# Performance work log

Hardware: AMD Instinct MI355X
Metric: run time of the kernel (lower is better)

Reference implementation:

```python
import jax, jax.numpy as jnp
import numpy as np

B, S, H = 1, 2000, 4096
NH, NKV, HD = 32, 8, 128
NREP = NH // NKV
ROPE_THETA = 10000.0
RES_LEN = 128          # kv_residual_len
K_BITS = V_BITS = 4
K_GROUP = V_GROUP = 64
NEG = -1e9


def setup_inputs() -> dict:
    key = jax.random.key(0)
    ks = jax.random.split(key, 6)
    hidden_states = jax.random.normal(ks[0], (B, S, H), jnp.float32) * 0.02
    wq = jax.random.normal(ks[1], (H, NH * HD), jnp.float32) * (H ** -0.5)
    wk = jax.random.normal(ks[2], (H, NKV * HD), jnp.float32) * (H ** -0.5)
    wv = jax.random.normal(ks[3], (H, NKV * HD), jnp.float32) * (H ** -0.5)
    wo = jax.random.normal(ks[4], (NH * HD, H), jnp.float32) * (H ** -0.5)
    position_ids = jnp.broadcast_to(jnp.arange(S, dtype=jnp.int64), (B, S))
    causal = jnp.tril(jnp.ones((S, S), dtype=bool))
    attention_mask = jnp.where(causal, 0.0, NEG).astype(jnp.float32)[None, None]  # [1,1,S,S]
    return {"hidden_states": hidden_states, "wq": wq, "wk": wk, "wv": wv,
            "wo": wo, "position_ids": position_ids, "attention_mask": attention_mask}


def _rotate_half(x):
    x1, x2 = jnp.split(x, 2, axis=-1)
    return jnp.concatenate([-x2, x1], axis=-1)


def _rope_cos_sin(position_ids):
    inv_freq = 1.0 / (ROPE_THETA ** (jnp.arange(0, HD, 2, dtype=jnp.float32) / HD))
    ang = position_ids.astype(jnp.float32)[..., None] * inv_freq  # [B,S,HD/2]
    emb = jnp.concatenate([ang, ang], axis=-1)                    # [B,S,HD]
    return jnp.cos(emb)[:, None], jnp.sin(emb)[:, None]           # [B,1,S,HD]


def _quant_dequant(x, bits, group):
    # group-wise asymmetric min/max fake-quant along head_dim
    sh = x.shape
    xg = x.reshape(sh[:-1] + (sh[-1] // group, group))
    mx = xg.max(axis=-1, keepdims=True)
    mn = xg.min(axis=-1, keepdims=True)
    scale = jnp.maximum((mx - mn) / (2 ** bits - 1), 1e-8)
    q = jnp.clip(jnp.round((xg - mn) / scale), 0, 2 ** bits - 1)
    return (q * scale + mn).reshape(sh)


def reference(hidden_states, wq, wk, wv, wo, position_ids, attention_mask):
    q = (hidden_states @ wq).reshape(B, S, NH, HD).transpose(0, 2, 1, 3)
    k = (hidden_states @ wk).reshape(B, S, NKV, HD).transpose(0, 2, 1, 3)
    v = (hidden_states @ wv).reshape(B, S, NKV, HD).transpose(0, 2, 1, 3)

    cos, sin = _rope_cos_sin(position_ids)
    q = q * cos + _rotate_half(q) * sin
    k = k * cos + _rotate_half(k) * sin

    # per-channel key stats (prefill path)
    k_scale = jnp.abs(k).max(axis=2, keepdims=True) ** 0.6  # [B,NKV,1,HD]
    k_bias = k.mean(axis=2, keepdims=True)                  # [B,NKV,1,HD]

    flen = S % RES_LEN  # residual tail kept in float
    if flen != 0:
        kq, kf = k[:, :, : S - flen], k[:, :, S - flen:]
        vq, vf = v[:, :, : S - flen], v[:, :, S - flen:]
    else:
        kq, kf, vq, vf = k, None, v, None

    # kv_quant_function: bias/scale-normalized key quant, plain value quant
    kh = (kq - k_bias) / k_scale
    kq = _quant_dequant(kh, K_BITS, K_GROUP) * k_scale + k_bias
    vq = _quant_dequant(vq, V_BITS, V_GROUP)

    k_full = jnp.concatenate([kq, kf], axis=2) if kf is not None else kq
    v_full = jnp.concatenate([vq, vf], axis=2) if vf is not None else vq

    k_full = jnp.repeat(k_full, NREP, axis=1)  # repeat_kv
    v_full = jnp.repeat(v_full, NREP, axis=1)

    attn = jnp.einsum("bhqd,bhkd->bhqk", q, k_full) / jnp.sqrt(jnp.float32(HD))
    attn = attn + attention_mask
    attn = jnp.maximum(attn, jnp.finfo(jnp.float32).min)
    w = jax.nn.softmax(attn.astype(jnp.float32), axis=-1).astype(q.dtype)
    out = jnp.einsum("bhqk,bhkd->bhqd", w, v_full)
    out = out.transpose(0, 2, 1, 3).reshape(B, S, NH * HD)
    return out @ wo
```

## Files before the change

### kernel.cpp

```cpp
#include <hip/hip_runtime.h>
#include <hip/hip_bf16.h>

#define S_LEN 2000
#define S_PAD 2048
#define NQKV 6144
#define QUANT_LEN 1920

typedef short short8 __attribute__((ext_vector_type(8)));
typedef float f32x4 __attribute__((ext_vector_type(4)));

__device__ __forceinline__ short f2b(float f) {
  unsigned u = __builtin_bit_cast(unsigned, f);
  u += 0x7fffu + ((u >> 16) & 1u);
  return (short)(u >> 16);
}
__device__ __forceinline__ float b2f(short s) {
  unsigned u = ((unsigned)(unsigned short)s) << 16;
  return __builtin_bit_cast(float, u);
}

__device__ __forceinline__ void gl_lds16(const void* g, void* lds) {
  __builtin_amdgcn_global_load_lds((__attribute__((address_space(1))) void*)(void*)g,
                                   (__attribute__((address_space(3))) void*)lds, 16, 0, 0);
}


__global__ __launch_bounds__(256) void cvt_hidden2(const float* __restrict__ src, short* __restrict__ hi,
                                                   short* __restrict__ lo) {
  long base = ((long)blockIdx.x * 256 + threadIdx.x) * 8;
  int row = (int)(base >> 12);
  short8 h, l;
  if (row < S_LEN) {
#pragma unroll
    for (int j = 0; j < 8; ++j) {
      float x = src[base + j];
      short hb = f2b(x);
      h[j] = hb;
      l[j] = f2b(x - b2f(hb));
    }
  } else {
#pragma unroll
    for (int j = 0; j < 8; ++j) { h[j] = 0; l[j] = 0; }
  }
  *(short8*)(hi + base) = h;
  *(short8*)(lo + base) = l;
}

__global__ __launch_bounds__(256) void transpose_cvt(const float* __restrict__ src, short* __restrict__ dst,
                                                     int K, int N) {
  __shared__ float t[32][33];
  int n0 = blockIdx.x * 32, k0 = blockIdx.y * 32;
  int tx = threadIdx.x & 31, ty = threadIdx.x >> 5;
#pragma unroll
  for (int i = 0; i < 4; ++i)
    t[ty + i * 8][tx] = src[(long)(k0 + ty + i * 8) * N + n0 + tx];
  __syncthreads();
#pragma unroll
  for (int i = 0; i < 4; ++i)
    dst[(long)(n0 + ty + i * 8) * K + k0 + tx] = f2b(t[tx][ty + i * 8]);
}

__global__ __launch_bounds__(256) void transpose_cvt2(const float* __restrict__ src, short* __restrict__ dhi,
                                                      short* __restrict__ dlo, int K, int N) {
  __shared__ float t[32][33];
  int n0 = blockIdx.x * 32, k0 = blockIdx.y * 32;
  int tx = threadIdx.x & 31, ty = threadIdx.x >> 5;
#pragma unroll
  for (int i = 0; i < 4; ++i)
    t[ty + i * 8][tx] = src[(long)(k0 + ty + i * 8) * N + n0 + tx];
  __syncthreads();
#pragma unroll
  for (int i = 0; i < 4; ++i) {
    float x = t[tx][ty + i * 8];
    short hb = f2b(x);
    long idx = (long)(n0 + ty + i * 8) * K + k0 + tx;
    dhi[idx] = hb;
    dlo[idx] = f2b(x - b2f(hb));
  }
}


__global__ __launch_bounds__(256, 2) void gemm_bt(const short* __restrict__ A, const short* __restrict__ BT,
                                                  float* __restrict__ C, int M_store, int ldc, int K) {
  __shared__ short As[128 * 64];
  __shared__ short Bs[128 * 64];
  int m0 = blockIdx.y * 128, n0 = blockIdx.x * 128;
  int t = threadIdx.x, lane = t & 63, w = t >> 6;
  int wm = w >> 1, wn = w & 1;
  int lr = lane & 15, lg = lane >> 4;
  int srow = lane >> 3, scol = (lane & 7) * 8;
  f32x4 acc[4][4];
#pragma unroll
  for (int mi = 0; mi < 4; ++mi)
#pragma unroll
    for (int ni = 0; ni < 4; ++ni) acc[mi][ni] = f32x4{0.f, 0.f, 0.f, 0.f};
  const int nk = K >> 6;
  const short* Ab = A + (long)(m0 + w * 32 + srow) * K + scol;
  const short* Bb = BT + (long)(n0 + w * 32 + srow) * K + scol;
  for (int kt = 0; kt < nk; ++kt) {
    __syncthreads();
#pragma unroll
    for (int j = 0; j < 4; ++j) {
      int c = w * 4 + j;
      gl_lds16(Ab + (long)j * 8 * K + kt * 64, &As[c * 512]);
      gl_lds16(Bb + (long)j * 8 * K + kt * 64, &Bs[c * 512]);
    }
    __syncthreads();
#pragma unroll
    for (int kk = 0; kk < 2; ++kk) {
      short8 a[4], b[4];
#pragma unroll
      for (int i = 0; i < 4; ++i) a[i] = *(const short8*)&As[(wm * 64 + i * 16 + lr) * 64 + kk * 32 + lg * 8];
#pragma unroll
      for (int i = 0; i < 4; ++i) b[i] = *(const short8*)&Bs[(wn * 64 + i * 16 + lr) * 64 + kk * 32 + lg * 8];
#pragma unroll
      for (int mi = 0; mi < 4; ++mi)
#pragma unroll
        for (int ni = 0; ni < 4; ++ni)
          acc[mi][ni] = __builtin_amdgcn_mfma_f32_16x16x32_bf16(a[mi], b[ni], acc[mi][ni], 0, 0, 0);
    }
  }
#pragma unroll
  for (int mi = 0; mi < 4; ++mi)
#pragma unroll
    for (int i = 0; i < 4; ++i) {
      int row = m0 + wm * 64 + mi * 16 + lg * 4 + i;
      if (row < M_store) {
#pragma unroll
        for (int ni = 0; ni < 4; ++ni)
          C[(long)row * ldc + n0 + wn * 64 + ni * 16 + lr] = acc[mi][ni][i];
      }
    }
}

__global__ __launch_bounds__(256, 1) void gemm_bt_split(const short* __restrict__ Ahi, const short* __restrict__ Alo,
                                                        const short* __restrict__ Bhi, const short* __restrict__ Blo,
                                                        float* __restrict__ C, int M_store, int ldc, int K) {
  __shared__ short Ash[128 * 64], Asl[128 * 64];
  __shared__ short Bsh[128 * 64], Bsl[128 * 64];
  int m0 = blockIdx.y * 128, n0 = blockIdx.x * 128;
  int t = threadIdx.x, lane = t & 63, w = t >> 6;
  int wm = w >> 1, wn = w & 1;
  int lr = lane & 15, lg = lane >> 4;
  int srow = lane >> 3, scol = (lane & 7) * 8;
  f32x4 acc[4][4];
#pragma unroll
  for (int mi = 0; mi < 4; ++mi)
#pragma unroll
    for (int ni = 0; ni < 4; ++ni) acc[mi][ni] = f32x4{0.f, 0.f, 0.f, 0.f};
  const int nk = K >> 6;
  long abase = (long)(m0 + w * 32 + srow) * K + scol;
  long bbase = (long)(n0 + w * 32 + srow) * K + scol;
  for (int kt = 0; kt < nk; ++kt) {
    __syncthreads();
#pragma unroll
    for (int j = 0; j < 4; ++j) {
      int c = w * 4 + j;
      long ao = abase + (long)j * 8 * K + kt * 64;
      long bo = bbase + (long)j * 8 * K + kt * 64;
      gl_lds16(Ahi + ao, &Ash[c * 512]);
      gl_lds16(Alo + ao, &Asl[c * 512]);
      gl_lds16(Bhi + bo, &Bsh[c * 512]);
      gl_lds16(Blo + bo, &Bsl[c * 512]);
    }
    __syncthreads();
#pragma unroll
    for (int kk = 0; kk < 2; ++kk) {
      short8 ah[4], al[4], bh[4], bl[4];
#pragma unroll
      for (int i = 0; i < 4; ++i) {
        int ro = (wm * 64 + i * 16 + lr) * 64 + kk * 32 + lg * 8;
        int co = (wn * 64 + i * 16 + lr) * 64 + kk * 32 + lg * 8;
        ah[i] = *(const short8*)&Ash[ro];
        al[i] = *(const short8*)&Asl[ro];
        bh[i] = *(const short8*)&Bsh[co];
        bl[i] = *(const short8*)&Bsl[co];
      }
#pragma unroll
      for (int mi = 0; mi < 4; ++mi)
#pragma unroll
        for (int ni = 0; ni < 4; ++ni) {
          acc[mi][ni] = __builtin_amdgcn_mfma_f32_16x16x32_bf16(ah[mi], bh[ni], acc[mi][ni], 0, 0, 0);
          acc[mi][ni] = __builtin_amdgcn_mfma_f32_16x16x32_bf16(ah[mi], bl[ni], acc[mi][ni], 0, 0, 0);
          acc[mi][ni] = __builtin_amdgcn_mfma_f32_16x16x32_bf16(al[mi], bh[ni], acc[mi][ni], 0, 0, 0);
        }
    }
  }
#pragma unroll
  for (int mi = 0; mi < 4; ++mi)
#pragma unroll
    for (int i = 0; i < 4; ++i) {
      int row = m0 + wm * 64 + mi * 16 + lg * 4 + i;
      if (row < M_store) {
#pragma unroll
        for (int ni = 0; ni < 4; ++ni)
          C[(long)row * ldc + n0 + wn * 64 + ni * 16 + lr] = acc[mi][ni][i];
      }
    }
}

__global__ __launch_bounds__(256) void rope_kernel(const float* __restrict__ qkv, short* __restrict__ qb,
                                                   float* __restrict__ kr) {
  __shared__ float invt[64];
  if (threadIdx.x < 64) invt[threadIdx.x] = (float)pow(10000.0, -(double)threadIdx.x / 64.0);
  __syncthreads();
  int s = blockIdx.x;
  bool valid = s < S_LEN;
  for (int p = threadIdx.x; p < 2560; p += 256) {
    int hh = p >> 6, j = p & 63;
    float ang = (float)s * invt[j];
    float c = cosf(ang), sn = sinf(ang);
    if (hh < 32) {
      long base = (long)s * NQKV + (long)hh * 128;
      float x1 = valid ? qkv[base + j] : 0.f;
      float x2 = valid ? qkv[base + j + 64] : 0.f;
      long ob = ((long)hh * S_PAD + s) * 128;
      qb[ob + j] = f2b(x1 * c - x2 * sn);
      qb[ob + j + 64] = f2b(x2 * c + x1 * sn);
    } else {
      int h = hh - 32;
      long base = (long)s * NQKV + 4096 + (long)h * 128;
      float x1 = valid ? qkv[base + j] : 0.f;
      float x2 = valid ? qkv[base + j + 64] : 0.f;
      long ob = ((long)h * S_PAD + s) * 128;
      kr[ob + j] = valid ? (x1 * c - x2 * sn) : 0.f;
      kr[ob + j + 64] = valid ? (x2 * c + x1 * sn) : 0.f;
    }
  }
}

__global__ __launch_bounds__(128) void kstat_partial(const float* __restrict__ kr, float* __restrict__ psum,
                                                     float* __restrict__ pmax) {
  int h = blockIdx.x, chunk = blockIdx.y, d = threadIdx.x;
  float sm = 0.f, mx = 0.f;
  int s0 = chunk * 100, s1 = s0 + 100;
  for (int s = s0; s < s1; ++s) {
    float v = kr[((long)h * S_PAD + s) * 128 + d];
    sm += v;
    mx = fmaxf(mx, fabsf(v));
  }
  psum[(h * 20 + chunk) * 128 + d] = sm;
  pmax[(h * 20 + chunk) * 128 + d] = mx;
}

__global__ __launch_bounds__(128) void kstat_final(const float* __restrict__ psum, const float* __restrict__ pmax,
                                                   float* __restrict__ bias, float* __restrict__ scale) {
  int h = blockIdx.x, d = threadIdx.x;
  float sm = 0.f, mx = 0.f;
  for (int c = 0; c < 20; ++c) {
    sm += psum[(h * 20 + c) * 128 + d];
    mx = fmaxf(mx, pmax[(h * 20 + c) * 128 + d]);
  }
  bias[h * 128 + d] = sm / 2000.0f;
  scale[h * 128 + d] = powf(mx, 0.6f);
}

__global__ __launch_bounds__(256) void quant_k(const float* __restrict__ kr, const float* __restrict__ bias,
                                               const float* __restrict__ scale, short* __restrict__ kb) {
  int gid = blockIdx.x * 4 + (threadIdx.x >> 6);
  int lane = threadIdx.x & 63;
  int h = gid >> 11, s = gid & 2047;
  long base = ((long)h * S_PAD + s) * 128;
  if (s >= S_LEN) {
    kb[base + lane] = 0;
    kb[base + lane + 64] = 0;
    return;
  }
  float x0 = kr[base + lane], x1 = kr[base + lane + 64];
  float o0, o1;
  if (s >= QUANT_LEN) {
    o0 = x0;
    o1 = x1;
  } else {
    float b0 = bias[h * 128 + lane], b1 = bias[h * 128 + lane + 64];
    float c0 = scale[h * 128 + lane], c1 = scale[h * 128 + lane + 64];
    float kh0 = (x0 - b0) / c0, kh1 = (x1 - b1) / c1;
    float mn0 = kh0, mx0 = kh0, mn1 = kh1, mx1 = kh1;
#pragma unroll
    for (int off = 1; off < 64; off <<= 1) {
      mn0 = fminf(mn0, __shfl_xor(mn0, off));
      mx0 = fmaxf(mx0, __shfl_xor(mx0, off));
      mn1 = fminf(mn1, __shfl_xor(mn1, off));
      mx1 = fmaxf(mx1, __shfl_xor(mx1, off));
    }
    float s0 = fmaxf((mx0 - mn0) / 15.f, 1e-8f), s1 = fmaxf((mx1 - mn1) / 15.f, 1e-8f);
    float q0 = fminf(fmaxf(rintf((kh0 - mn0) / s0), 0.f), 15.f);
    float q1 = fminf(fmaxf(rintf((kh1 - mn1) / s1), 0.f), 15.f);
    o0 = (q0 * s0 + mn0) * c0 + b0;
    o1 = (q1 * s1 + mn1) * c1 + b1;
  }
  kb[base + lane] = f2b(o0);
  kb[base + lane + 64] = f2b(o1);
}

__global__ __launch_bounds__(256) void quant_v(const float* __restrict__ qkv, short* __restrict__ vt) {
  int gid = blockIdx.x * 4 + (threadIdx.x >> 6);
  int lane = threadIdx.x & 63;
  int h = gid >> 11, s = gid & 2047;
  float o0 = 0.f, o1 = 0.f;
  if (s < S_LEN) {
    long base = (long)s * NQKV + 5120 + (long)h * 128;
    float x0 = qkv[base + lane], x1 = qkv[base + lane + 64];
    if (s >= QUANT_LEN) {
      o0 = x0;
      o1 = x1;
    } else {
      float mn0 = x0, mx0 = x0, mn1 = x1, mx1 = x1;
#pragma unroll
      for (int off = 1; off < 64; off <<= 1) {
        mn0 = fminf(mn0, __shfl_xor(mn0, off));
        mx0 = fmaxf(mx0, __shfl_xor(mx0, off));
        mn1 = fminf(mn1, __shfl_xor(mn1, off));
        mx1 = fmaxf(mx1, __shfl_xor(mx1, off));
      }
      float s0 = fmaxf((mx0 - mn0) / 15.f, 1e-8f), s1 = fmaxf((mx1 - mn1) / 15.f, 1e-8f);
      float q0 = fminf(fmaxf(rintf((x0 - mn0) / s0), 0.f), 15.f);
      float q1 = fminf(fmaxf(rintf((x1 - mn1) / s1), 0.f), 15.f);
      o0 = q0 * s0 + mn0;
      o1 = q1 * s1 + mn1;
    }
  }
  long ob = (long)h * 128 * S_PAD;
  vt[ob + (long)lane * S_PAD + s] = f2b(o0);
  vt[ob + (long)(lane + 64) * S_PAD + s] = f2b(o1);
}


__global__ __launch_bounds__(256) void flash_attn(const short* __restrict__ qb, const short* __restrict__ kb,
                                                  const short* __restrict__ vt, short* __restrict__ ao) {
  __shared__ short Ks[64][136];
  __shared__ short Vs[128][72];
  __shared__ short Ps[4][16][72];
  int bx = blockIdx.x;
  int qt = 31 - (bx >> 5);
  int h = bx & 31;
  int kvh = h >> 2;
  int t = threadIdx.x, lane = t & 63, w = t >> 6;
  int lr = lane & 15, lg = lane >> 4;
  int qrow = qt * 64 + w * 16;
  short8 qf[4];
#pragma unroll
  for (int kk = 0; kk < 4; ++kk)
    qf[kk] = *(const short8*)(qb + ((long)h * S_PAD + qrow + lr) * 128 + kk * 32 + lg * 8);
  f32x4 o[8];
#pragma unroll
  for (int nb = 0; nb < 8; ++nb) o[nb] = f32x4{0.f, 0.f, 0.f, 0.f};
  float m_i[4], l_i[4];
#pragma unroll
  for (int i = 0; i < 4; ++i) {
    m_i[i] = -1e30f;
    l_i[i] = 0.f;
  }
  const float sm_scale = 0.08838834764831845f;
  int nkt = qt + 1;
  for (int kt = 0; kt < nkt; ++kt) {
    __syncthreads();
    {
      int r = t >> 2, cc = (t & 3) * 32;
      const short* src = kb + ((long)kvh * S_PAD + kt * 64 + r) * 128 + cc;
#pragma unroll
      for (int j = 0; j < 4; ++j) *(short8*)&Ks[r][cc + j * 8] = *(const short8*)(src + j * 8);
    }
    {
      int d = t >> 1, cc = (t & 1) * 32;
      const short* src = vt + ((long)kvh * 128 + d) * S_PAD + kt * 64 + cc;
#pragma unroll
      for (int j = 0; j < 4; ++j) *(short8*)&Vs[d][cc + j * 8] = *(const short8*)(src + j * 8);
    }
    __syncthreads();
    f32x4 sc[4];
#pragma unroll
    for (int nb = 0; nb < 4; ++nb) sc[nb] = f32x4{0.f, 0.f, 0.f, 0.f};
    __builtin_amdgcn_s_setprio(1);
#pragma unroll
    for (int kk = 0; kk < 4; ++kk) {
#pragma unroll
      for (int nb = 0; nb < 4; ++nb) {
        short8 bk = *(const short8*)&Ks[nb * 16 + lr][kk * 32 + lg * 8];
        sc[nb] = __builtin_amdgcn_mfma_f32_16x16x32_bf16(qf[kk], bk, sc[nb], 0, 0, 0);
      }
    }
    __builtin_amdgcn_s_setprio(0);
    float mrow[4];
#pragma unroll
    for (int i = 0; i < 4; ++i) mrow[i] = -1e30f;
#pragma unroll
    for (int nb = 0; nb < 4; ++nb) {
      int key = kt * 64 + nb * 16 + lr;
#pragma unroll
      for (int i = 0; i < 4; ++i) {
        int qr = qrow + lg * 4 + i;
        float v = sc[nb][i] * sm_scale + (key > qr ? -1e9f : 0.f);
        sc[nb][i] = v;
        mrow[i] = fmaxf(mrow[i], v);
      }
    }
#pragma unroll
    for (int off = 1; off < 16; off <<= 1)
#pragma unroll
      for (int i = 0; i < 4; ++i) mrow[i] = fmaxf(mrow[i], __shfl_xor(mrow[i], off));
    float mnew[4], fac[4], rsum[4];
#pragma unroll
    for (int i = 0; i < 4; ++i) {
      mnew[i] = fmaxf(m_i[i], mrow[i]);
      fac[i] = __expf(m_i[i] - mnew[i]);
      m_i[i] = mnew[i];
      rsum[i] = 0.f;
    }
#pragma unroll
    for (int nb = 0; nb < 4; ++nb)
#pragma unroll
      for (int i = 0; i < 4; ++i) {
        float p = __expf(sc[nb][i] - mnew[i]);
        sc[nb][i] = p;
        rsum[i] += p;
      }
#pragma unroll
    for (int off = 1; off < 16; off <<= 1)
#pragma unroll
      for (int i = 0; i < 4; ++i) rsum[i] += __shfl_xor(rsum[i], off);
#pragma unroll
    for (int i = 0; i < 4; ++i) l_i[i] = l_i[i] * fac[i] + rsum[i];
#pragma unroll
    for (int nb = 0; nb < 8; ++nb)
#pragma unroll
      for (int i = 0; i < 4; ++i) o[nb][i] *= fac[i];
#pragma unroll
    for (int nb = 0; nb < 4; ++nb)
#pragma unroll
      for (int i = 0; i < 4; ++i) Ps[w][lg * 4 + i][nb * 16 + lr] = f2b(sc[nb][i]);
    __builtin_amdgcn_s_setprio(1);
#pragma unroll
    for (int kkk = 0; kkk < 2; ++kkk) {
      short8 pa = *(const short8*)&Ps[w][lr][kkk * 32 + lg * 8];
#pragma unroll
      for (int nb = 0; nb < 8; ++nb) {
        short8 bv = *(const short8*)&Vs[nb * 16 + lr][kkk * 32 + lg * 8];
        o[nb] = __builtin_amdgcn_mfma_f32_16x16x32_bf16(pa, bv, o[nb], 0, 0, 0);
      }
    }
    __builtin_amdgcn_s_setprio(0);
  }
  float linv[4];
#pragma unroll
  for (int i = 0; i < 4; ++i) linv[i] = 1.0f / l_i[i];
#pragma unroll
  for (int nb = 0; nb < 8; ++nb)
#pragma unroll
    for (int i = 0; i < 4; ++i) {
      int s = qrow + lg * 4 + i;
      ao[(long)s * 4096 + h * 128 + nb * 16 + lr] = f2b(o[nb][i] * linv[i]);
    }
}


extern "C" void kernel_launch(void* const* d_in, const int* in_sizes, int n_in,
                              void* d_out, int out_size, void* d_ws, size_t ws_size,
                              hipStream_t stream) {
  const float* hidden = (const float*)d_in[0];
  const float* wq = (const float*)d_in[1];
  const float* wk = (const float*)d_in[2];
  const float* wv = (const float*)d_in[3];
  const float* wo = (const float*)d_in[4];
  float* out = (float*)d_out;
  char* ws = (char*)d_ws;
  size_t off = 0;
  auto alloc = [&](size_t bytes) -> void* {
    void* p = ws + off;
    off += (bytes + 255) & ~(size_t)255;
    return p;
  };
  short* wqT = (short*)alloc(4096L * 4096 * 2);
  short* wkvT_hi = (short*)alloc(2048L * 4096 * 2);
  short* wkvT_lo = (short*)alloc(2048L * 4096 * 2);
  float* qkvf = (float*)alloc(2048L * 6144 * 4);
  short* hb_hi = (short*)alloc(2048L * 4096 * 2);
  short* hb_lo = (short*)alloc(2048L * 4096 * 2);
  short* qb2 = (short*)alloc(32L * 2048 * 128 * 2);
  float* kr = (float*)alloc(8L * 2048 * 128 * 4);
  short* kbq = (short*)alloc(8L * 2048 * 128 * 2);
  short* vt = (short*)alloc(8L * 128 * 2048 * 2);
  float* psum = (float*)alloc(8L * 20 * 128 * 4);
  float* pmax = (float*)alloc(8L * 20 * 128 * 4);
  float* kbias = (float*)alloc(1024 * 4);
  float* kscale = (float*)alloc(1024 * 4);
  short* woT = (short*)qkvf;
  short* ab = hb_hi;

  cvt_hidden2<<<4096, 256, 0, stream>>>(hidden, hb_hi, hb_lo);
  transpose_cvt<<<dim3(128, 128), 256, 0, stream>>>(wq, wqT, 4096, 4096);
  transpose_cvt2<<<dim3(32, 128), 256, 0, stream>>>(wk, wkvT_hi, wkvT_lo, 4096, 1024);
  transpose_cvt2<<<dim3(32, 128), 256, 0, stream>>>(wv, wkvT_hi + 1024L * 4096, wkvT_lo + 1024L * 4096, 4096, 1024);
  gemm_bt<<<dim3(32, 16), 256, 0, stream>>>(hb_hi, wqT, qkvf, 2000, 6144, 4096);
  gemm_bt_split<<<dim3(16, 16), 256, 0, stream>>>(hb_hi, hb_lo, wkvT_hi, wkvT_lo, qkvf + 4096, 2000, 6144, 4096);
  rope_kernel<<<2048, 256, 0, stream>>>(qkvf, qb2, kr);
  kstat_partial<<<dim3(8, 20), 128, 0, stream>>>(kr, psum, pmax);
  kstat_final<<<8, 128, 0, stream>>>(psum, pmax, kbias, kscale);
  quant_k<<<4096, 256, 0, stream>>>(kr, kbias, kscale, kbq);
  quant_v<<<4096, 256, 0, stream>>>(qkvf, vt);
  transpose_cvt<<<dim3(128, 128), 256, 0, stream>>>(wo, woT, 4096, 4096);
  flash_attn<<<1024, 256, 0, stream>>>(qb2, kbq, vt, ab);
  gemm_bt<<<dim3(32, 16), 256, 0, stream>>>(ab, woT, out, 2000, 4096, 4096);
}
```

Baseline: 680.5 us.

## Fold K projection into plain bf16 Q GEMM and split-K the V GEMM

The K projection moves out of the three-MFMA hi/lo split GEMM and is appended to the single-bf16 Q GEMM, which now produces a 5120-wide output. The remaining split-precision V GEMM is split four ways along K to launch more blocks, and quant_v sums the four partial outputs. The wo transpose is moved earlier, which is safe because quant_v no longer reads the aliased qkv buffer. This removes a third of the expensive split MFMA work for K, but K now carries plain bf16 error into its quantization, and the V path adds extra partial-buffer traffic.

```diff
diff --git a/kernel.cpp b/kernel.cpp
--- a/kernel.cpp
+++ b/kernel.cpp
@@ -3,7 +3,7 @@
 
 #define S_LEN 2000
 #define S_PAD 2048
-#define NQKV 6144
+#define QKN 5120
 #define QUANT_LEN 1920
 
 typedef short short8 __attribute__((ext_vector_type(8)));
@@ -135,10 +135,11 @@
 
 __global__ __launch_bounds__(256, 1) void gemm_bt_split(const short* __restrict__ Ahi, const short* __restrict__ Alo,
                                                         const short* __restrict__ Bhi, const short* __restrict__ Blo,
-                                                        float* __restrict__ C, int M_store, int ldc, int K) {
+                                                        float* __restrict__ Cpart, int M_store, int Ktot, int Kslice) {
   __shared__ short Ash[128 * 64], Asl[128 * 64];
   __shared__ short Bsh[128 * 64], Bsl[128 * 64];
   int m0 = blockIdx.y * 128, n0 = blockIdx.x * 128;
+  int bz = blockIdx.z;
   int t = threadIdx.x, lane = t & 63, w = t >> 6;
   int wm = w >> 1, wn = w & 1;
   int lr = lane & 15, lg = lane >> 4;
@@ -148,16 +149,17 @@
   for (int mi = 0; mi < 4; ++mi)
 #pragma unroll
     for (int ni = 0; ni < 4; ++ni) acc[mi][ni] = f32x4{0.f, 0.f, 0.f, 0.f};
-  const int nk = K >> 6;
-  long abase = (long)(m0 + w * 32 + srow) * K + scol;
-  long bbase = (long)(n0 + w * 32 + srow) * K + scol;
+  const int nk = Kslice >> 6;
+  long abase = (long)(m0 + w * 32 + srow) * Ktot + (long)bz * Kslice + scol;
+  long bbase = (long)(n0 + w * 32 + srow) * Ktot + (long)bz * Kslice + scol;
+  float* C = Cpart + (long)bz * 2048 * 1024;
   for (int kt = 0; kt < nk; ++kt) {
     __syncthreads();
 #pragma unroll
     for (int j = 0; j < 4; ++j) {
       int c = w * 4 + j;
-      long ao = abase + (long)j * 8 * K + kt * 64;
-      long bo = bbase + (long)j * 8 * K + kt * 64;
+      long ao = abase + (long)j * 8 * Ktot + kt * 64;
+      long bo = bbase + (long)j * 8 * Ktot + kt * 64;
       gl_lds16(Ahi + ao, &Ash[c * 512]);
       gl_lds16(Alo + ao, &Asl[c * 512]);
       gl_lds16(Bhi + bo, &Bsh[c * 512]);
@@ -194,7 +196,7 @@
       if (row < M_store) {
 #pragma unroll
         for (int ni = 0; ni < 4; ++ni)
-          C[(long)row * ldc + n0 + wn * 64 + ni * 16 + lr] = acc[mi][ni][i];
+          C[(long)row * 1024 + n0 + wn * 64 + ni * 16 + lr] = acc[mi][ni][i];
       }
     }
 }
@@ -211,7 +213,7 @@
     float ang = (float)s * invt[j];
     float c = cosf(ang), sn = sinf(ang);
     if (hh < 32) {
-      long base = (long)s * NQKV + (long)hh * 128;
+      long base = (long)s * QKN + (long)hh * 128;
       float x1 = valid ? qkv[base + j] : 0.f;
       float x2 = valid ? qkv[base + j + 64] : 0.f;
       long ob = ((long)hh * S_PAD + s) * 128;
@@ -219,7 +221,7 @@
       qb[ob + j + 64] = f2b(x2 * c + x1 * sn);
     } else {
       int h = hh - 32;
-      long base = (long)s * NQKV + 4096 + (long)h * 128;
+      long base = (long)s * QKN + 4096 + (long)h * 128;
       float x1 = valid ? qkv[base + j] : 0.f;
       float x2 = valid ? qkv[base + j + 64] : 0.f;
       long ob = ((long)h * S_PAD + s) * 128;
@@ -293,14 +295,16 @@
   kb[base + lane + 64] = f2b(o1);
 }
 
-__global__ __launch_bounds__(256) void quant_v(const float* __restrict__ qkv, short* __restrict__ vt) {
+__global__ __launch_bounds__(256) void quant_v(const float* __restrict__ vp, short* __restrict__ vt) {
   int gid = blockIdx.x * 4 + (threadIdx.x >> 6);
   int lane = threadIdx.x & 63;
   int h = gid >> 11, s = gid & 2047;
   float o0 = 0.f, o1 = 0.f;
   if (s < S_LEN) {
-    long base = (long)s * NQKV + 5120 + (long)h * 128;
-    float x0 = qkv[base + lane], x1 = qkv[base + lane + 64];
+    long b = (long)s * 1024 + h * 128;
+    const long PS = 2048L * 1024;
+    float x0 = vp[b + lane] + vp[PS + b + lane] + vp[2 * PS + b + lane] + vp[3 * PS + b + lane];
+    float x1 = vp[b + lane + 64] + vp[PS + b + lane + 64] + vp[2 * PS + b + lane + 64] + vp[3 * PS + b + lane + 64];
     if (s >= QUANT_LEN) {
       o0 = x0;
       o1 = x1;
@@ -470,10 +474,11 @@
     off += (bytes + 255) & ~(size_t)255;
     return p;
   };
-  short* wqT = (short*)alloc(4096L * 4096 * 2);
-  short* wkvT_hi = (short*)alloc(2048L * 4096 * 2);
-  short* wkvT_lo = (short*)alloc(2048L * 4096 * 2);
-  float* qkvf = (float*)alloc(2048L * 6144 * 4);
+  short* wqkT = (short*)alloc(5120L * 4096 * 2);
+  short* wvT_hi = (short*)alloc(1024L * 4096 * 2);
+  short* wvT_lo = (short*)alloc(1024L * 4096 * 2);
+  float* qkvf = (float*)alloc(2048L * 5120 * 4);
+  float* vpart = (float*)alloc(4L * 2048 * 1024 * 4);
   short* hb_hi = (short*)alloc(2048L * 4096 * 2);
   short* hb_lo = (short*)alloc(2048L * 4096 * 2);
   short* qb2 = (short*)alloc(32L * 2048 * 128 * 2);
@@ -488,17 +493,17 @@
   short* ab = hb_hi;
 
   cvt_hidden2<<<4096, 256, 0, stream>>>(hidden, hb_hi, hb_lo);
-  transpose_cvt<<<dim3(128, 128), 256, 0, stream>>>(wq, wqT, 4096, 4096);
-  transpose_cvt2<<<dim3(32, 128), 256, 0, stream>>>(wk, wkvT_hi, wkvT_lo, 4096, 1024);
-  transpose_cvt2<<<dim3(32, 128), 256, 0, stream>>>(wv, wkvT_hi + 1024L * 4096, wkvT_lo + 1024L * 4096, 4096, 1024);
-  gemm_bt<<<dim3(32, 16), 256, 0, stream>>>(hb_hi, wqT, qkvf, 2000, 6144, 4096);
-  gemm_bt_split<<<dim3(16, 16), 256, 0, stream>>>(hb_hi, hb_lo, wkvT_hi, wkvT_lo, qkvf + 4096, 2000, 6144, 4096);
+  transpose_cvt<<<dim3(128, 128), 256, 0, stream>>>(wq, wqkT, 4096, 4096);
+  transpose_cvt<<<dim3(32, 128), 256, 0, stream>>>(wk, wqkT + 4096L * 4096, 4096, 1024);
+  transpose_cvt2<<<dim3(32, 128), 256, 0, stream>>>(wv, wvT_hi, wvT_lo, 4096, 1024);
+  gemm_bt<<<dim3(40, 16), 256, 0, stream>>>(hb_hi, wqkT, qkvf, 2000, 5120, 4096);
+  gemm_bt_split<<<dim3(8, 16, 4), 256, 0, stream>>>(hb_hi, hb_lo, wvT_hi, wvT_lo, vpart, 2000, 4096, 1024);
   rope_kernel<<<2048, 256, 0, stream>>>(qkvf, qb2, kr);
+  transpose_cvt<<<dim3(128, 128), 256, 0, stream>>>(wo, woT, 4096, 4096);
   kstat_partial<<<dim3(8, 20), 128, 0, stream>>>(kr, psum, pmax);
   kstat_final<<<8, 128, 0, stream>>>(psum, pmax, kbias, kscale);
   quant_k<<<4096, 256, 0, stream>>>(kr, kbias, kscale, kbq);
-  quant_v<<<4096, 256, 0, stream>>>(qkvf, vt);
-  transpose_cvt<<<dim3(128, 128), 256, 0, stream>>>(wo, woT, 4096, 4096);
+  quant_v<<<4096, 256, 0, stream>>>(vpart, vt);
   flash_attn<<<1024, 256, 0, stream>>>(qb2, kbq, vt, ab);
   gemm_bt<<<dim3(32, 16), 256, 0, stream>>>(ab, woT, out, 2000, 4096, 4096);
 }
```

Result: faster. 616.2 us (-9.4%).
